# Kernel optimization log

Measured on AMD Instinct MI355X. Metric: run time of the kernel, lower is better.

The kernel has to match this reference:

```python
import jax, jax.numpy as jnp
import numpy as np

B, T, I, H, L, O = 32, 512, 256, 512, 2, 128

def setup_inputs() -> dict:
    key = jax.random.key(0)
    ks = jax.random.split(key, 11)
    s_i = 1.0 / np.sqrt(H)
    inp = {"x": jax.random.normal(ks[0], (B, T, I), jnp.float32)}
    for l in range(L):
        in_dim = I if l == 0 else H
        inp[f"W_ih_{l}"] = jax.random.uniform(ks[1 + 4 * l], (3 * H, in_dim), jnp.float32, -s_i, s_i)
        inp[f"W_hh_{l}"] = jax.random.uniform(ks[2 + 4 * l], (3 * H, H), jnp.float32, -s_i, s_i)
        inp[f"b_ih_{l}"] = jax.random.uniform(ks[3 + 4 * l], (3 * H,), jnp.float32, -s_i, s_i)
        inp[f"b_hh_{l}"] = jax.random.uniform(ks[4 + 4 * l], (3 * H,), jnp.float32, -s_i, s_i)
    inp["fc_W"] = jax.random.uniform(ks[9], (O, H), jnp.float32, -s_i, s_i)
    inp["fc_b"] = jax.random.uniform(ks[10], (O,), jnp.float32, -s_i, s_i)
    return inp

def _gru_layer(x, W_ih, W_hh, b_ih, b_hh):
    # x: [B,T,in] -> precompute input projections once (big batched GEMM)
    xp = jnp.einsum('bti,gi->btg', x, W_ih) + b_ih  # [B,T,3H]
    h0 = jnp.zeros((x.shape[0], W_hh.shape[1]), x.dtype)
    def step(h, xt):  # xt: [B,3H]
        gh = h @ W_hh.T + b_hh  # [B,3H]
        xr, xz, xn = jnp.split(xt, 3, axis=-1)
        hr, hz, hn = jnp.split(gh, 3, axis=-1)
        r = jax.nn.sigmoid(xr + hr)
        z = jax.nn.sigmoid(xz + hz)
        n = jnp.tanh(xn + r * hn)
        h_new = (1.0 - z) * n + z * h
        return h_new, h_new
    hT, ys = jax.lax.scan(step, h0, jnp.swapaxes(xp, 0, 1))  # ys: [T,B,H]
    return jnp.swapaxes(ys, 0, 1), hT

def reference(x, W_ih_0, W_hh_0, b_ih_0, b_hh_0, W_ih_1, W_hh_1, b_ih_1, b_hh_1, fc_W, fc_b):
    layers = [(W_ih_0, W_hh_0, b_ih_0, b_hh_0), (W_ih_1, W_hh_1, b_ih_1, b_hh_1)]
    h = x
    finals = []
    for (Wi, Wh, bi, bh) in layers:
        h, hT = _gru_layer(h, Wi, Wh, bi, bh)
        finals.append(hT)
    hidden = jnp.stack(finals, axis=0)  # [L,B,H]
    out = jnp.einsum('bth,oh->bto', h, fc_W) + fc_b  # [B,T,O]
    return out, hidden
```

## Files before the change

### kernel.cpp

```cpp
#include <hip/hip_runtime.h>
#include <math.h>

#define Bsz 32
#define Tt  512
#define Isz 256
#define Hsz 512
#define G3  1536
#define Osz 128

#define NBLK 256
#define TPB  512
#define G0_L0 1u
#define G0_L1 4096u
#define POLL_GUARD (1 << 22)

typedef float f4  __attribute__((ext_vector_type(4)));
typedef float f32x4 __attribute__((ext_vector_type(4)));
typedef _Float16 half8_t __attribute__((ext_vector_type(8)));
typedef _Float16 half4_t __attribute__((ext_vector_type(4)));
typedef unsigned int u32;
typedef u32 u32x2 __attribute__((ext_vector_type(2)));

__device__ __forceinline__ float sigf(float x) { return 1.0f / (1.0f + expf(-x)); }

__global__ void f32_to_f16(const float* __restrict__ in, _Float16* __restrict__ out, int n4) {
    int i = threadIdx.x + blockIdx.x * blockDim.x;
    int stride = blockDim.x * gridDim.x;
    for (int k = i; k < n4; k += stride) {
        float4 v = reinterpret_cast<const float4*>(in)[k];
        half4_t o;
        o[0] = (_Float16)v.x; o[1] = (_Float16)v.y;
        o[2] = (_Float16)v.z; o[3] = (_Float16)v.w;
        reinterpret_cast<half4_t*>(out)[k] = o;
    }
}

__global__ void init_pbuf(u32x2* pbuf, u32 gen0) {
    int i = threadIdx.x + blockIdx.x * blockDim.x;
    const int n = Bsz * Hsz;
    for (; i < n; i += gridDim.x * blockDim.x) {
        pbuf[i]     = (u32x2){0u, gen0};
        pbuf[n + i] = (u32x2){0u, 0u};
    }
}

__global__ void __launch_bounds__(TPB, 2) gru_rec(
    const float* __restrict__ xp,
    const float* __restrict__ Whh,
    const float* __restrict__ bhh,
    float* __restrict__ hall,
    u32x2* __restrict__ pbuf,
    float* __restrict__ hid_out,
    u32 g0)
{
    const int tid = threadIdx.x;
    const int b   = blockIdx.x & 31;
    const int p   = blockIdx.x >> 5;
    const int jl  = tid >> 3;
    const int kc  = tid & 7;
    const int j   = p * 64 + jl;

    __shared__ float hsh[8 * 68];

    f4 wreg[3][16];
    #pragma unroll
    for (int g = 0; g < 3; ++g) {
        const float* wp = Whh + (size_t)(g * Hsz + j) * Hsz + kc * 64;
        #pragma unroll
        for (int q = 0; q < 16; ++q)
            wreg[g][q] = *reinterpret_cast<const f4*>(wp + q * 4);
    }
    #pragma unroll
    for (int g = 0; g < 3; ++g)
        #pragma unroll
        for (int q = 0; q < 16; ++q)
            asm volatile("" : "+v"(wreg[g][q]));

    const float bh0 = bhh[0 * Hsz + j];
    const float bh1 = bhh[1 * Hsz + j];
    const float bh2 = bhh[2 * Hsz + j];

    for (int t = 0; t < Tt; ++t) {
        const u32 rg = g0 + (u32)t;
        const u32 wg = rg + 1u;
        const u32x2* src = pbuf + (size_t)(t & 1) * (Bsz * Hsz) + b * Hsz;
        u32x2*       dst = pbuf + (size_t)((t + 1) & 1) * (Bsz * Hsz) + b * Hsz;

        float xr = 0.f, xz = 0.f, xn = 0.f;
        if (kc == 0) {
            const float* pp = xp + (size_t)(b * Tt + t) * G3;
            xr = pp[j];
            xz = pp[Hsz + j];
            xn = pp[2 * Hsz + j];
        }

        {
            const u32x2* sp = src + tid;
            int guard = 0;
            for (;;) {
                u32x2 pr;
                asm volatile("global_load_dwordx2 %0, %1, off sc0 sc1\n\t"
                             "s_waitcnt vmcnt(0)"
                             : "=&v"(pr) : "v"(sp) : "memory");
                if (__all(pr[1] == rg) || ++guard > POLL_GUARD) {
                    hsh[(tid >> 6) * 68 + (tid & 63)] = __uint_as_float(pr[0]);
                    break;
                }
                __builtin_amdgcn_s_sleep(1);
            }
        }
        __syncthreads();

        float a0 = 0.f, a1 = 0.f, a2 = 0.f;
        {
            const f4* hp = reinterpret_cast<const f4*>(hsh) + kc * 17;
            #pragma unroll
            for (int q = 0; q < 16; ++q) {
                f4 hv4 = hp[q];
                a0 = fmaf(wreg[0][q][0], hv4[0], a0);
                a0 = fmaf(wreg[0][q][1], hv4[1], a0);
                a0 = fmaf(wreg[0][q][2], hv4[2], a0);
                a0 = fmaf(wreg[0][q][3], hv4[3], a0);
                a1 = fmaf(wreg[1][q][0], hv4[0], a1);
                a1 = fmaf(wreg[1][q][1], hv4[1], a1);
                a1 = fmaf(wreg[1][q][2], hv4[2], a1);
                a1 = fmaf(wreg[1][q][3], hv4[3], a1);
                a2 = fmaf(wreg[2][q][0], hv4[0], a2);
                a2 = fmaf(wreg[2][q][1], hv4[1], a2);
                a2 = fmaf(wreg[2][q][2], hv4[2], a2);
                a2 = fmaf(wreg[2][q][3], hv4[3], a2);
            }
        }

        #pragma unroll
        for (int off = 1; off < 8; off <<= 1) {
            a0 += __shfl_xor(a0, off, 64);
            a1 += __shfl_xor(a1, off, 64);
            a2 += __shfl_xor(a2, off, 64);
        }

        if (kc == 0) {
            float rr = sigf(xr + a0 + bh0);
            float zz = sigf(xz + a1 + bh1);
            float nn = tanhf(xn + rr * (a2 + bh2));
            float ho = hsh[(j >> 6) * 68 + (j & 63)];
            float hv = (1.0f - zz) * nn + zz * ho;
            u32x2 pk = (u32x2){__float_as_uint(hv), wg};
            asm volatile("global_store_dwordx2 %0, %1, off sc0 sc1"
                         :: "v"(dst + j), "v"(pk) : "memory");
            hall[(size_t)(b * Tt + t) * Hsz + j] = hv;
            if (t == Tt - 1) hid_out[b * Hsz + j] = hv;
        }

        __syncthreads();
    }
}

__global__ void __launch_bounds__(256) gemm_nt_mfma(
    const float* __restrict__ A,
    const _Float16* __restrict__ Wh,
    const float* __restrict__ bias,
    float* __restrict__ C,
    int M, int N, int K)
{
    const int tid = threadIdx.x;
    const int l   = tid & 63;
    const int w   = tid >> 6;
    const int wm  = w >> 1, wn = w & 1;
    const int m0  = blockIdx.y * 128 + wm * 64;
    const int n0  = blockIdx.x * 128 + wn * 64;
    const int lr  = l & 15;
    const int lk  = (l >> 4) * 8;

    f32x4 acc[4][4];
    #pragma unroll
    for (int mt = 0; mt < 4; ++mt)
        #pragma unroll
        for (int nt = 0; nt < 4; ++nt)
            acc[mt][nt] = (f32x4){0.f, 0.f, 0.f, 0.f};

    for (int ks = 0; ks < K; ks += 32) {
        half8_t af[4], bf[4];
        #pragma unroll
        for (int mt = 0; mt < 4; ++mt) {
            const float* pa = A + (size_t)(m0 + mt * 16 + lr) * K + ks + lk;
            float4 v0 = *reinterpret_cast<const float4*>(pa);
            float4 v1 = *reinterpret_cast<const float4*>(pa + 4);
            half8_t h;
            h[0] = (_Float16)v0.x; h[1] = (_Float16)v0.y;
            h[2] = (_Float16)v0.z; h[3] = (_Float16)v0.w;
            h[4] = (_Float16)v1.x; h[5] = (_Float16)v1.y;
            h[6] = (_Float16)v1.z; h[7] = (_Float16)v1.w;
            af[mt] = h;
        }
        #pragma unroll
        for (int nt = 0; nt < 4; ++nt)
            bf[nt] = *reinterpret_cast<const half8_t*>(Wh + (size_t)(n0 + nt * 16 + lr) * K + ks + lk);
        #pragma unroll
        for (int mt = 0; mt < 4; ++mt)
            #pragma unroll
            for (int nt = 0; nt < 4; ++nt)
                acc[mt][nt] = __builtin_amdgcn_mfma_f32_16x16x32_f16(af[mt], bf[nt], acc[mt][nt], 0, 0, 0);
    }

    #pragma unroll
    for (int nt = 0; nt < 4; ++nt) {
        const int colg = n0 + nt * 16 + lr;
        const float bb = bias[colg];
        #pragma unroll
        for (int mt = 0; mt < 4; ++mt) {
            #pragma unroll
            for (int r = 0; r < 4; ++r) {
                int rowg = m0 + mt * 16 + (l >> 4) * 4 + r;
                C[(size_t)rowg * N + colg] = acc[mt][nt][r] + bb;
            }
        }
    }
}

#define GM 64
#define GN 64
#define GK 16
__global__ void __launch_bounds__(256) gemm_nt_bias(
    const float* __restrict__ A, const float* __restrict__ W,
    const float* __restrict__ bias, float* __restrict__ C,
    int M, int N, int K)
{
    __shared__ float As[GK][GM];
    __shared__ float Bs[GK][GN];
    const int tid = threadIdx.x;
    const int n0 = blockIdx.x * GN;
    const int m0 = blockIdx.y * GM;
    const int tn = tid & 15;
    const int tm = tid >> 4;
    const int lrow = tid >> 2;
    const int lkq  = tid & 3;

    float acc[4][4];
    #pragma unroll
    for (int i = 0; i < 4; ++i)
        #pragma unroll
        for (int jj = 0; jj < 4; ++jj) acc[i][jj] = 0.0f;

    for (int k0 = 0; k0 < K; k0 += GK) {
        float4 av = *reinterpret_cast<const float4*>(&A[(size_t)(m0 + lrow) * K + k0 + lkq * 4]);
        float4 wv = *reinterpret_cast<const float4*>(&W[(size_t)(n0 + lrow) * K + k0 + lkq * 4]);
        __syncthreads();
        As[lkq * 4 + 0][lrow] = av.x; As[lkq * 4 + 1][lrow] = av.y;
        As[lkq * 4 + 2][lrow] = av.z; As[lkq * 4 + 3][lrow] = av.w;
        Bs[lkq * 4 + 0][lrow] = wv.x; Bs[lkq * 4 + 1][lrow] = wv.y;
        Bs[lkq * 4 + 2][lrow] = wv.z; Bs[lkq * 4 + 3][lrow] = wv.w;
        __syncthreads();
        #pragma unroll
        for (int k = 0; k < GK; ++k) {
            float4 a4 = *reinterpret_cast<const float4*>(&As[k][tm * 4]);
            float4 b4 = *reinterpret_cast<const float4*>(&Bs[k][tn * 4]);
            acc[0][0] = fmaf(a4.x, b4.x, acc[0][0]); acc[0][1] = fmaf(a4.x, b4.y, acc[0][1]);
            acc[0][2] = fmaf(a4.x, b4.z, acc[0][2]); acc[0][3] = fmaf(a4.x, b4.w, acc[0][3]);
            acc[1][0] = fmaf(a4.y, b4.x, acc[1][0]); acc[1][1] = fmaf(a4.y, b4.y, acc[1][1]);
            acc[1][2] = fmaf(a4.y, b4.z, acc[1][2]); acc[1][3] = fmaf(a4.y, b4.w, acc[1][3]);
            acc[2][0] = fmaf(a4.z, b4.x, acc[2][0]); acc[2][1] = fmaf(a4.z, b4.y, acc[2][1]);
            acc[2][2] = fmaf(a4.z, b4.z, acc[2][2]); acc[2][3] = fmaf(a4.z, b4.w, acc[2][3]);
            acc[3][0] = fmaf(a4.w, b4.x, acc[3][0]); acc[3][1] = fmaf(a4.w, b4.y, acc[3][1]);
            acc[3][2] = fmaf(a4.w, b4.z, acc[3][2]); acc[3][3] = fmaf(a4.w, b4.w, acc[3][3]);
        }
    }

    float4 bb = *reinterpret_cast<const float4*>(&bias[n0 + tn * 4]);
    #pragma unroll
    for (int i = 0; i < 4; ++i) {
        int m = m0 + tm * 4 + i;
        float4 o;
        o.x = acc[i][0] + bb.x; o.y = acc[i][1] + bb.y;
        o.z = acc[i][2] + bb.z; o.w = acc[i][3] + bb.w;
        *reinterpret_cast<float4*>(&C[(size_t)m * N + n0 + tn * 4]) = o;
    }
}

extern "C" void kernel_launch(void* const* d_in, const int* in_sizes, int n_in,
                              void* d_out, int out_size, void* d_ws, size_t ws_size,
                              hipStream_t stream) {
    (void)in_sizes; (void)n_in; (void)out_size; (void)ws_size;
    const float* x    = (const float*)d_in[0];
    const float* Wih0 = (const float*)d_in[1];
    const float* Whh0 = (const float*)d_in[2];
    const float* bih0 = (const float*)d_in[3];
    const float* bhh0 = (const float*)d_in[4];
    const float* Wih1 = (const float*)d_in[5];
    const float* Whh1 = (const float*)d_in[6];
    const float* bih1 = (const float*)d_in[7];
    const float* bhh1 = (const float*)d_in[8];
    const float* fcW  = (const float*)d_in[9];
    const float* fcb  = (const float*)d_in[10];

    float* out = (float*)d_out;
    float* hid = out + (size_t)Bsz * Tt * Osz;

    char* ws = (char*)d_ws;
    const size_t xp_off   = 0;
    const size_t hall_off = xp_off + (size_t)Bsz * Tt * G3 * 4;
    const size_t pbuf_off = hall_off + (size_t)Bsz * Tt * Hsz * 4;
    const size_t w0h_off  = pbuf_off + (size_t)2 * Bsz * Hsz * 8;
    const size_t w1h_off  = w0h_off + (size_t)G3 * Isz * 2;
    float*     xp    = (float*)(ws + xp_off);
    float*     hall  = (float*)(ws + hall_off);
    u32x2*     pbuf  = (u32x2*)(ws + pbuf_off);
    _Float16*  W0h   = (_Float16*)(ws + w0h_off);
    _Float16*  W1h   = (_Float16*)(ws + w1h_off);

    hipLaunchKernelGGL(f32_to_f16, dim3(128), dim3(256), 0, stream, Wih0, W0h, G3 * Isz / 4);
    hipLaunchKernelGGL(f32_to_f16, dim3(256), dim3(256), 0, stream, Wih1, W1h, G3 * Hsz / 4);

    hipLaunchKernelGGL(gemm_nt_mfma, dim3(G3 / 128, (Bsz * Tt) / 128), dim3(256), 0, stream,
                       x, W0h, bih0, xp, Bsz * Tt, G3, Isz);

    hipLaunchKernelGGL(init_pbuf, dim3(64), dim3(256), 0, stream, pbuf, G0_L0);
    hipLaunchKernelGGL(gru_rec, dim3(NBLK), dim3(TPB), 0, stream,
                       xp, Whh0, bhh0, hall, pbuf, hid, G0_L0);

    hipLaunchKernelGGL(gemm_nt_mfma, dim3(G3 / 128, (Bsz * Tt) / 128), dim3(256), 0, stream,
                       hall, W1h, bih1, xp, Bsz * Tt, G3, Hsz);

    hipLaunchKernelGGL(init_pbuf, dim3(64), dim3(256), 0, stream, pbuf, G0_L1);
    hipLaunchKernelGGL(gru_rec, dim3(NBLK), dim3(TPB), 0, stream,
                       xp, Whh1, bhh1, hall, pbuf, hid + Bsz * Hsz, G0_L1);

    hipLaunchKernelGGL(gemm_nt_bias, dim3(Osz / GN, (Bsz * Tt) / GM), dim3(256), 0, stream,
                       hall, fcW, fcb, out, Bsz * Tt, Osz, Hsz);
}
```

Baseline: 1.978 ms.

## Process two batch rows per block with half the hidden slice

```diff
diff --git a/kernel.cpp b/kernel.cpp
--- a/kernel.cpp
+++ b/kernel.cpp
@@ -13,6 +13,7 @@
 #define G0_L0 1u
 #define G0_L1 4096u
 #define POLL_GUARD (1 << 22)
+#define CH 36
 
 typedef float f4  __attribute__((ext_vector_type(4)));
 typedef float f32x4 __attribute__((ext_vector_type(4)));
@@ -53,57 +54,66 @@
     float* __restrict__ hid_out,
     u32 g0)
 {
-    const int tid = threadIdx.x;
-    const int b   = blockIdx.x & 31;
-    const int p   = blockIdx.x >> 5;
-    const int jl  = tid >> 3;
-    const int kc  = tid & 7;
-    const int j   = p * 64 + jl;
-
-    __shared__ float hsh[8 * 68];
-
-    f4 wreg[3][16];
+    const int tid  = threadIdx.x;
+    const int pr   = blockIdx.x & 15;
+    const int p    = blockIdx.x >> 4;
+    const int b1   = pr * 2;
+    const int b2   = b1 + 1;
+    const int jl   = tid >> 4;
+    const int kc   = tid & 15;
+    const int j    = p * 32 + jl;
+    const int BH   = Bsz * Hsz;
+
+    __shared__ float hA[16 * CH];
+    __shared__ float hB[16 * CH];
+
+    f4 wreg[3][8];
     #pragma unroll
     for (int g = 0; g < 3; ++g) {
-        const float* wp = Whh + (size_t)(g * Hsz + j) * Hsz + kc * 64;
-        #pragma unroll
-        for (int q = 0; q < 16; ++q)
+        const float* wp = Whh + (size_t)(g * Hsz + j) * Hsz + kc * 32;
+        #pragma unroll
+        for (int q = 0; q < 8; ++q)
             wreg[g][q] = *reinterpret_cast<const f4*>(wp + q * 4);
     }
     #pragma unroll
     for (int g = 0; g < 3; ++g)
         #pragma unroll
-        for (int q = 0; q < 16; ++q)
+        for (int q = 0; q < 8; ++q)
             asm volatile("" : "+v"(wreg[g][q]));
 
     const float bh0 = bhh[0 * Hsz + j];
     const float bh1 = bhh[1 * Hsz + j];
     const float bh2 = bhh[2 * Hsz + j];
 
+    const int li = (tid >> 5) * CH + (tid & 31);
+    const int lo = (j >> 5) * CH + (j & 31);
+
     for (int t = 0; t < Tt; ++t) {
         const u32 rg = g0 + (u32)t;
         const u32 wg = rg + 1u;
-        const u32x2* src = pbuf + (size_t)(t & 1) * (Bsz * Hsz) + b * Hsz;
-        u32x2*       dst = pbuf + (size_t)((t + 1) & 1) * (Bsz * Hsz) + b * Hsz;
-
-        float xr = 0.f, xz = 0.f, xn = 0.f;
+        const u32x2* srcA = pbuf + (size_t)(t & 1) * BH + b1 * Hsz;
+        u32x2*       dstA = pbuf + (size_t)((t + 1) & 1) * BH + b1 * Hsz;
+        const u32x2* srcB = pbuf + (size_t)(t & 1) * BH + b2 * Hsz;
+        u32x2*       dstB = pbuf + (size_t)((t + 1) & 1) * BH + b2 * Hsz;
+
+        float xrA = 0.f, xzA = 0.f, xnA = 0.f, xrB = 0.f, xzB = 0.f, xnB = 0.f;
         if (kc == 0) {
-            const float* pp = xp + (size_t)(b * Tt + t) * G3;
-            xr = pp[j];
-            xz = pp[Hsz + j];
-            xn = pp[2 * Hsz + j];
+            const float* pA = xp + (size_t)(b1 * Tt + t) * G3;
+            const float* pB = xp + (size_t)(b2 * Tt + t) * G3;
+            xrA = pA[j]; xzA = pA[Hsz + j]; xnA = pA[2 * Hsz + j];
+            xrB = pB[j]; xzB = pB[Hsz + j]; xnB = pB[2 * Hsz + j];
         }
 
         {
-            const u32x2* sp = src + tid;
+            const u32x2* sp = srcA + tid;
             int guard = 0;
             for (;;) {
-                u32x2 pr;
+                u32x2 prv;
                 asm volatile("global_load_dwordx2 %0, %1, off sc0 sc1\n\t"
                              "s_waitcnt vmcnt(0)"
-                             : "=&v"(pr) : "v"(sp) : "memory");
-                if (__all(pr[1] == rg) || ++guard > POLL_GUARD) {
-                    hsh[(tid >> 6) * 68 + (tid & 63)] = __uint_as_float(pr[0]);
+                             : "=&v"(prv) : "v"(sp) : "memory");
+                if (__all(prv[1] == rg) || ++guard > POLL_GUARD) {
+                    hA[li] = __uint_as_float(prv[0]);
                     break;
                 }
                 __builtin_amdgcn_s_sleep(1);
@@ -111,11 +121,11 @@
         }
         __syncthreads();
 
-        float a0 = 0.f, a1 = 0.f, a2 = 0.f;
         {
-            const f4* hp = reinterpret_cast<const f4*>(hsh) + kc * 17;
-            #pragma unroll
-            for (int q = 0; q < 16; ++q) {
+            float a0 = 0.f, a1 = 0.f, a2 = 0.f;
+            const f4* hp = reinterpret_cast<const f4*>(hA + kc * CH);
+            #pragma unroll
+            for (int q = 0; q < 8; ++q) {
                 f4 hv4 = hp[q];
                 a0 = fmaf(wreg[0][q][0], hv4[0], a0);
                 a0 = fmaf(wreg[0][q][1], hv4[1], a0);
@@ -130,29 +140,81 @@
                 a2 = fmaf(wreg[2][q][2], hv4[2], a2);
                 a2 = fmaf(wreg[2][q][3], hv4[3], a2);
             }
-        }
-
-        #pragma unroll
-        for (int off = 1; off < 8; off <<= 1) {
-            a0 += __shfl_xor(a0, off, 64);
-            a1 += __shfl_xor(a1, off, 64);
-            a2 += __shfl_xor(a2, off, 64);
-        }
-
-        if (kc == 0) {
-            float rr = sigf(xr + a0 + bh0);
-            float zz = sigf(xz + a1 + bh1);
-            float nn = tanhf(xn + rr * (a2 + bh2));
-            float ho = hsh[(j >> 6) * 68 + (j & 63)];
-            float hv = (1.0f - zz) * nn + zz * ho;
-            u32x2 pk = (u32x2){__float_as_uint(hv), wg};
-            asm volatile("global_store_dwordx2 %0, %1, off sc0 sc1"
-                         :: "v"(dst + j), "v"(pk) : "memory");
-            hall[(size_t)(b * Tt + t) * Hsz + j] = hv;
-            if (t == Tt - 1) hid_out[b * Hsz + j] = hv;
-        }
-
+            #pragma unroll
+            for (int off = 1; off < 16; off <<= 1) {
+                a0 += __shfl_xor(a0, off, 64);
+                a1 += __shfl_xor(a1, off, 64);
+                a2 += __shfl_xor(a2, off, 64);
+            }
+            if (kc == 0) {
+                float rr = sigf(xrA + a0 + bh0);
+                float zz = sigf(xzA + a1 + bh1);
+                float nn = tanhf(xnA + rr * (a2 + bh2));
+                float ho = hA[lo];
+                float hv = (1.0f - zz) * nn + zz * ho;
+                u32x2 pk = (u32x2){__float_as_uint(hv), wg};
+                asm volatile("global_store_dwordx2 %0, %1, off sc0 sc1"
+                             :: "v"(dstA + j), "v"(pk) : "memory");
+                hall[(size_t)(b1 * Tt + t) * Hsz + j] = hv;
+                if (t == Tt - 1) hid_out[b1 * Hsz + j] = hv;
+            }
+        }
+
+        {
+            const u32x2* sp = srcB + tid;
+            int guard = 0;
+            for (;;) {
+                u32x2 prv;
+                asm volatile("global_load_dwordx2 %0, %1, off sc0 sc1\n\t"
+                             "s_waitcnt vmcnt(0)"
+                             : "=&v"(prv) : "v"(sp) : "memory");
+                if (__all(prv[1] == rg) || ++guard > POLL_GUARD) {
+                    hB[li] = __uint_as_float(prv[0]);
+                    break;
+                }
+                __builtin_amdgcn_s_sleep(1);
+            }
+        }
         __syncthreads();
+
+        {
+            float a0 = 0.f, a1 = 0.f, a2 = 0.f;
+            const f4* hp = reinterpret_cast<const f4*>(hB + kc * CH);
+            #pragma unroll
+            for (int q = 0; q < 8; ++q) {
+                f4 hv4 = hp[q];
+                a0 = fmaf(wreg[0][q][0], hv4[0], a0);
+                a0 = fmaf(wreg[0][q][1], hv4[1], a0);
+                a0 = fmaf(wreg[0][q][2], hv4[2], a0);
+                a0 = fmaf(wreg[0][q][3], hv4[3], a0);
+                a1 = fmaf(wreg[1][q][0], hv4[0], a1);
+                a1 = fmaf(wreg[1][q][1], hv4[1], a1);
+                a1 = fmaf(wreg[1][q][2], hv4[2], a1);
+                a1 = fmaf(wreg[1][q][3], hv4[3], a1);
+                a2 = fmaf(wreg[2][q][0], hv4[0], a2);
+                a2 = fmaf(wreg[2][q][1], hv4[1], a2);
+                a2 = fmaf(wreg[2][q][2], hv4[2], a2);
+                a2 = fmaf(wreg[2][q][3], hv4[3], a2);
+            }
+            #pragma unroll
+            for (int off = 1; off < 16; off <<= 1) {
+                a0 += __shfl_xor(a0, off, 64);
+                a1 += __shfl_xor(a1, off, 64);
+                a2 += __shfl_xor(a2, off, 64);
+            }
+            if (kc == 0) {
+                float rr = sigf(xrB + a0 + bh0);
+                float zz = sigf(xzB + a1 + bh1);
+                float nn = tanhf(xnB + rr * (a2 + bh2));
+                float ho = hB[lo];
+                float hv = (1.0f - zz) * nn + zz * ho;
+                u32x2 pk = (u32x2){__float_as_uint(hv), wg};
+                asm volatile("global_store_dwordx2 %0, %1, off sc0 sc1"
+                             :: "v"(dstB + j), "v"(pk) : "memory");
+                hall[(size_t)(b2 * Tt + t) * Hsz + j] = hv;
+                if (t == Tt - 1) hid_out[b2 * Hsz + j] = hv;
+            }
+        }
     }
 }
 
```

Measured after the change: 3.033 ms. 53.4% more time.

## Fuse both GRU layers into one wavefront-pipelined persistent kernel

Applied to the files above, without the earlier changes.

```diff
diff --git a/kernel.cpp b/kernel.cpp
--- a/kernel.cpp
+++ b/kernel.cpp
@@ -8,18 +8,19 @@
 #define G3  1536
 #define Osz 128
 
-#define NBLK 256
 #define TPB  512
-#define G0_L0 1u
-#define G0_L1 4096u
+#define NFUSED 192
 #define POLL_GUARD (1 << 22)
-
-typedef float f4  __attribute__((ext_vector_type(4)));
+#define BH  (Bsz * Hsz)
+#define XQP (Bsz * G3)
+
+typedef float f4 __attribute__((ext_vector_type(4)));
 typedef float f32x4 __attribute__((ext_vector_type(4)));
 typedef _Float16 half8_t __attribute__((ext_vector_type(8)));
 typedef _Float16 half4_t __attribute__((ext_vector_type(4)));
 typedef unsigned int u32;
 typedef u32 u32x2 __attribute__((ext_vector_type(2)));
+typedef u32 u32x4 __attribute__((ext_vector_type(4)));
 
 __device__ __forceinline__ float sigf(float x) { return 1.0f / (1.0f + expf(-x)); }
 
@@ -35,132 +36,397 @@
     }
 }
 
-__global__ void init_pbuf(u32x2* pbuf, u32 gen0) {
+__global__ void init_bufs(u32x2* pbuf0, u32x2* pbuf1, u32x2* xqbuf,
+                          int* prog0, int* prog1) {
     int i = threadIdx.x + blockIdx.x * blockDim.x;
-    const int n = Bsz * Hsz;
-    for (; i < n; i += gridDim.x * blockDim.x) {
-        pbuf[i]     = (u32x2){0u, gen0};
-        pbuf[n + i] = (u32x2){0u, 0u};
+    int stride = blockDim.x * gridDim.x;
+    for (int k = i; k < 8 * BH; k += stride)
+        pbuf0[k] = (k < BH) ? (u32x2){0u, 1u} : (u32x2){0u, 0u};
+    for (int k = i; k < 2 * BH; k += stride)
+        pbuf1[k] = (k < BH) ? (u32x2){0u, 1u} : (u32x2){0u, 0u};
+    for (int k = i; k < 8 * XQP; k += stride)
+        xqbuf[k] = (u32x2){0u, 0u};
+    for (int k = i; k < 1024; k += stride) { prog0[k] = 0; prog1[k] = 0; }
+}
+
+__global__ void __launch_bounds__(TPB, 1) gru_fused(
+    const float* __restrict__ xp,
+    const float* __restrict__ Whh0, const float* __restrict__ bhh0,
+    const float* __restrict__ Wih1, const float* __restrict__ bih1,
+    const float* __restrict__ Whh1, const float* __restrict__ bhh1,
+    float* __restrict__ hall,
+    u32x2* __restrict__ pbuf0,
+    u32x2* __restrict__ pbuf1,
+    u32x2* __restrict__ xqbuf,
+    int* __restrict__ prog0,
+    int* __restrict__ prog1,
+    float* __restrict__ hid)
+{
+    const int tid  = threadIdx.x;
+    const int rid  = blockIdx.x;
+    const int role = rid >> 6;
+    const int loc  = rid & 63;
+    const int bg   = loc >> 3;
+    const int p    = loc & 7;
+    const int jl   = tid >> 3;
+    const int kc   = tid & 7;
+    const int j    = p * 64 + jl;
+    const int li   = (tid >> 6) * 68 + (tid & 63);
+    const int lo   = (j >> 6) * 68 + (j & 63);
+
+    __shared__ float hs[4 * 544];
+
+    if (role == 0) {
+        f4 w[3][16];
+        #pragma unroll
+        for (int g = 0; g < 3; ++g) {
+            const float* wp = Whh0 + (size_t)(g * Hsz + j) * Hsz + kc * 64;
+            #pragma unroll
+            for (int q = 0; q < 16; ++q) w[g][q] = *reinterpret_cast<const f4*>(wp + q * 4);
+        }
+        #pragma unroll
+        for (int g = 0; g < 3; ++g)
+            #pragma unroll
+            for (int q = 0; q < 16; ++q) asm volatile("" : "+v"(w[g][q]));
+        const float b0 = bhh0[j], b1 = bhh0[Hsz + j], b2 = bhh0[2 * Hsz + j];
+        int bpk = 0;
+
+        for (int t = 0; t < Tt; ++t) {
+            const u32 rg = (u32)(t + 1), wgen = rg + 1u;
+            const u32x2* src = pbuf0 + (size_t)(t & 7) * BH + bg * 4 * Hsz;
+            u32x2*       dst = pbuf0 + (size_t)((t + 1) & 7) * BH + bg * 4 * Hsz;
+
+            float xr[4], xz[4], xn[4];
+            if (kc == 0) {
+                #pragma unroll
+                for (int bi = 0; bi < 4; ++bi) {
+                    const float* pp = xp + (size_t)((bg * 4 + bi) * Tt + t) * G3;
+                    xr[bi] = pp[j]; xz[bi] = pp[Hsz + j]; xn[bi] = pp[2 * Hsz + j];
+                }
+            }
+
+            {
+                const u32x2* a0 = src + 0 * Hsz + tid;
+                const u32x2* a1 = src + 1 * Hsz + tid;
+                const u32x2* a2 = src + 2 * Hsz + tid;
+                const u32x2* a3 = src + 3 * Hsz + tid;
+                u32x2 r0, r1, r2, r3;
+                int guard = 0;
+                for (;;) {
+                    asm volatile(
+                        "global_load_dwordx2 %0, %4, off sc0 sc1\n\t"
+                        "global_load_dwordx2 %1, %5, off sc0 sc1\n\t"
+                        "global_load_dwordx2 %2, %6, off sc0 sc1\n\t"
+                        "global_load_dwordx2 %3, %7, off sc0 sc1\n\t"
+                        "s_waitcnt vmcnt(0)"
+                        : "=&v"(r0), "=&v"(r1), "=&v"(r2), "=&v"(r3)
+                        : "v"(a0), "v"(a1), "v"(a2), "v"(a3) : "memory");
+                    bool ok = (r0[1] == rg) && (r1[1] == rg) && (r2[1] == rg) && (r3[1] == rg);
+                    if (__all(ok) || ++guard > POLL_GUARD) break;
+                    __builtin_amdgcn_s_sleep(1);
+                }
+                hs[0 * 544 + li] = __uint_as_float(r0[0]);
+                hs[1 * 544 + li] = __uint_as_float(r1[0]);
+                hs[2 * 544 + li] = __uint_as_float(r2[0]);
+                hs[3 * 544 + li] = __uint_as_float(r3[0]);
+            }
+            __syncthreads();
+
+            {
+                const int thr = t - 7;
+                if (tid < 64 && thr > bpk) {
+                    const int* pp = prog0 + ((bg << 3) + (tid & 7)) * 16;
+                    int guard = 0;
+                    for (;;) {
+                        int v;
+                        asm volatile("global_load_dword %0, %1, off sc0 sc1\n\t"
+                                     "s_waitcnt vmcnt(0)" : "=&v"(v) : "v"(pp) : "memory");
+                        int mv = (tid < 8) ? v : 0x7fffffff;
+                        #pragma unroll
+                        for (int off = 1; off < 8; off <<= 1) {
+                            int o = __shfl_xor(mv, off, 64);
+                            mv = (o < mv) ? o : mv;
+                        }
+                        mv = __shfl(mv, 0, 64);
+                        if (mv >= thr || ++guard > POLL_GUARD) { bpk = mv; break; }
+                        __builtin_amdgcn_s_sleep(2);
+                    }
+                }
+            }
+            __syncthreads();
+
+            #pragma unroll
+            for (int bi = 0; bi < 4; ++bi) {
+                float a0 = 0.f, a1 = 0.f, a2 = 0.f;
+                const f4* hp = reinterpret_cast<const f4*>(hs + bi * 544) + kc * 17;
+                #pragma unroll
+                for (int q = 0; q < 16; ++q) {
+                    f4 hv4 = hp[q];
+                    a0 = fmaf(w[0][q][0], hv4[0], a0); a0 = fmaf(w[0][q][1], hv4[1], a0);
+                    a0 = fmaf(w[0][q][2], hv4[2], a0); a0 = fmaf(w[0][q][3], hv4[3], a0);
+                    a1 = fmaf(w[1][q][0], hv4[0], a1); a1 = fmaf(w[1][q][1], hv4[1], a1);
+                    a1 = fmaf(w[1][q][2], hv4[2], a1); a1 = fmaf(w[1][q][3], hv4[3], a1);
+                    a2 = fmaf(w[2][q][0], hv4[0], a2); a2 = fmaf(w[2][q][1], hv4[1], a2);
+                    a2 = fmaf(w[2][q][2], hv4[2], a2); a2 = fmaf(w[2][q][3], hv4[3], a2);
+                }
+                #pragma unroll
+                for (int off = 1; off < 8; off <<= 1) {
+                    a0 += __shfl_xor(a0, off, 64);
+                    a1 += __shfl_xor(a1, off, 64);
+                    a2 += __shfl_xor(a2, off, 64);
+                }
+                if (kc == 0) {
+                    float rr = sigf(xr[bi] + a0 + b0);
+                    float zz = sigf(xz[bi] + a1 + b1);
+                    float nn = tanhf(xn[bi] + rr * (a2 + b2));
+                    float ho = hs[bi * 544 + lo];
+                    float hv = (1.0f - zz) * nn + zz * ho;
+                    u32x2 pk = (u32x2){__float_as_uint(hv), wgen};
+                    asm volatile("global_store_dwordx2 %0, %1, off sc0 sc1"
+                                 :: "v"(dst + bi * Hsz + j), "v"(pk) : "memory");
+                    if (t == Tt - 1) hid[(bg * 4 + bi) * Hsz + j] = hv;
+                }
+            }
+            __syncthreads();
+        }
+    } else if (role == 1) {
+        f4 w[3][16];
+        #pragma unroll
+        for (int g = 0; g < 3; ++g) {
+            const float* wp = Wih1 + (size_t)(g * Hsz + j) * Hsz + kc * 64;
+            #pragma unroll
+            for (int q = 0; q < 16; ++q) w[g][q] = *reinterpret_cast<const f4*>(wp + q * 4);
+        }
+        #pragma unroll
+        for (int g = 0; g < 3; ++g)
+            #pragma unroll
+            for (int q = 0; q < 16; ++q) asm volatile("" : "+v"(w[g][q]));
+        const float b0 = bih1[j], b1 = bih1[Hsz + j], b2 = bih1[2 * Hsz + j];
+        int bpk = 0;
+
+        for (int t = 0; t < Tt; ++t) {
+            const u32 rgp = (u32)(t + 2);
+            const u32x2* src = pbuf0 + (size_t)((t + 1) & 7) * BH + bg * 4 * Hsz;
+            u32x2* xdst = xqbuf + (size_t)((t + 1) & 7) * XQP;
+
+            {
+                const u32x2* a0 = src + 0 * Hsz + tid;
+                const u32x2* a1 = src + 1 * Hsz + tid;
+                const u32x2* a2 = src + 2 * Hsz + tid;
+                const u32x2* a3 = src + 3 * Hsz + tid;
+                u32x2 r0, r1, r2, r3;
+                int guard = 0;
+                for (;;) {
+                    asm volatile(
+                        "global_load_dwordx2 %0, %4, off sc0 sc1\n\t"
+                        "global_load_dwordx2 %1, %5, off sc0 sc1\n\t"
+                        "global_load_dwordx2 %2, %6, off sc0 sc1\n\t"
+                        "global_load_dwordx2 %3, %7, off sc0 sc1\n\t"
+                        "s_waitcnt vmcnt(0)"
+                        : "=&v"(r0), "=&v"(r1), "=&v"(r2), "=&v"(r3)
+                        : "v"(a0), "v"(a1), "v"(a2), "v"(a3) : "memory");
+                    bool ok = (r0[1] == rgp) && (r1[1] == rgp) && (r2[1] == rgp) && (r3[1] == rgp);
+                    if (__all(ok) || ++guard > POLL_GUARD) break;
+                    __builtin_amdgcn_s_sleep(1);
+                }
+                hs[0 * 544 + li] = __uint_as_float(r0[0]);
+                hs[1 * 544 + li] = __uint_as_float(r1[0]);
+                hs[2 * 544 + li] = __uint_as_float(r2[0]);
+                hs[3 * 544 + li] = __uint_as_float(r3[0]);
+            }
+            __syncthreads();
+
+            if (tid == 0) {
+                int pv = t + 1;
+                asm volatile("global_store_dword %0, %1, off sc0 sc1"
+                             :: "v"(prog0 + ((bg << 3) + p) * 16), "v"(pv) : "memory");
+                const int thr = t - 7;
+                if (thr > bpk) {
+                    const int* pp = prog1 + ((bg << 3) + p) * 16;
+                    int guard = 0;
+                    for (;;) {
+                        int v;
+                        asm volatile("global_load_dword %0, %1, off sc0 sc1\n\t"
+                                     "s_waitcnt vmcnt(0)" : "=&v"(v) : "v"(pp) : "memory");
+                        if (v >= thr || ++guard > POLL_GUARD) { bpk = v; break; }
+                        __builtin_amdgcn_s_sleep(2);
+                    }
+                }
+            }
+            __syncthreads();
+
+            #pragma unroll
+            for (int bi = 0; bi < 4; ++bi) {
+                float a0 = 0.f, a1 = 0.f, a2 = 0.f;
+                const f4* hp = reinterpret_cast<const f4*>(hs + bi * 544) + kc * 17;
+                #pragma unroll
+                for (int q = 0; q < 16; ++q) {
+                    f4 hv4 = hp[q];
+                    a0 = fmaf(w[0][q][0], hv4[0], a0); a0 = fmaf(w[0][q][1], hv4[1], a0);
+                    a0 = fmaf(w[0][q][2], hv4[2], a0); a0 = fmaf(w[0][q][3], hv4[3], a0);
+                    a1 = fmaf(w[1][q][0], hv4[0], a1); a1 = fmaf(w[1][q][1], hv4[1], a1);
+                    a1 = fmaf(w[1][q][2], hv4[2], a1); a1 = fmaf(w[1][q][3], hv4[3], a1);
+                    a2 = fmaf(w[2][q][0], hv4[0], a2); a2 = fmaf(w[2][q][1], hv4[1], a2);
+                    a2 = fmaf(w[2][q][2], hv4[2], a2); a2 = fmaf(w[2][q][3], hv4[3], a2);
+                }
+                #pragma unroll
+                for (int off = 1; off < 8; off <<= 1) {
+                    a0 += __shfl_xor(a0, off, 64);
+                    a1 += __shfl_xor(a1, off, 64);
+                    a2 += __shfl_xor(a2, off, 64);
+                }
+                if (kc == 0) {
+                    float v0 = a0 + b0, v1 = a1 + b1, v2 = a2 + b2;
+                    u32x4 pk0 = (u32x4){__float_as_uint(v0), rgp, __float_as_uint(v1), rgp};
+                    u32x2 pk1 = (u32x2){__float_as_uint(v2), rgp};
+                    u32x2* xa = xdst + (size_t)((bg * 4 + bi) * Hsz + j) * 3;
+                    asm volatile(
+                        "global_store_dwordx4 %0, %1, off sc0 sc1\n\t"
+                        "global_store_dwordx2 %0, %2, off offset:16 sc0 sc1"
+                        :: "v"(xa), "v"(pk0), "v"(pk1) : "memory");
+                }
+            }
+            __syncthreads();
+        }
+    } else {
+        f4 w[3][16];
+        #pragma unroll
+        for (int g = 0; g < 3; ++g) {
+            const float* wp = Whh1 + (size_t)(g * Hsz + j) * Hsz + kc * 64;
+            #pragma unroll
+            for (int q = 0; q < 16; ++q) w[g][q] = *reinterpret_cast<const f4*>(wp + q * 4);
+        }
+        #pragma unroll
+        for (int g = 0; g < 3; ++g)
+            #pragma unroll
+            for (int q = 0; q < 16; ++q) asm volatile("" : "+v"(w[g][q]));
+        const float b0 = bhh1[j], b1 = bhh1[Hsz + j], b2 = bhh1[2 * Hsz + j];
+
+        for (int t = 0; t < Tt; ++t) {
+            const u32 rg = (u32)(t + 1), wgen = rg + 1u, rgx = rg + 1u;
+            const u32x2* src = pbuf1 + (size_t)(t & 1) * BH + bg * 4 * Hsz;
+            u32x2*       dst = pbuf1 + (size_t)((t + 1) & 1) * BH + bg * 4 * Hsz;
+            const u32x2* xsrc = xqbuf + (size_t)((t + 1) & 7) * XQP;
+
+            u32x4 xa_[4]; u32x2 xb_[4];
+            const u32x2* xaddr[4];
+            #pragma unroll
+            for (int bi = 0; bi < 4; ++bi)
+                xaddr[bi] = xsrc + (size_t)((bg * 4 + bi) * Hsz + j) * 3;
+            if (kc == 0) {
+                #pragma unroll
+                for (int bi = 0; bi < 4; ++bi)
+                    asm volatile(
+                        "global_load_dwordx4 %0, %2, off sc0 sc1\n\t"
+                        "global_load_dwordx2 %1, %2, off offset:16 sc0 sc1"
+                        : "=&v"(xa_[bi]), "=&v"(xb_[bi]) : "v"(xaddr[bi]) : "memory");
+            }
+
+            {
+                const u32x2* a0 = src + 0 * Hsz + tid;
+                const u32x2* a1 = src + 1 * Hsz + tid;
+                const u32x2* a2 = src + 2 * Hsz + tid;
+                const u32x2* a3 = src + 3 * Hsz + tid;
+                u32x2 r0, r1, r2, r3;
+                int guard = 0;
+                for (;;) {
+                    asm volatile(
+                        "global_load_dwordx2 %0, %4, off sc0 sc1\n\t"
+                        "global_load_dwordx2 %1, %5, off sc0 sc1\n\t"
+                        "global_load_dwordx2 %2, %6, off sc0 sc1\n\t"
+                        "global_load_dwordx2 %3, %7, off sc0 sc1\n\t"
+                        "s_waitcnt vmcnt(0)"
+                        : "=&v"(r0), "=&v"(r1), "=&v"(r2), "=&v"(r3)
+                        : "v"(a0), "v"(a1), "v"(a2), "v"(a3) : "memory");
+                    bool ok = (r0[1] == rg) && (r1[1] == rg) && (r2[1] == rg) && (r3[1] == rg);
+                    if (__all(ok) || ++guard > POLL_GUARD) break;
+                    __builtin_amdgcn_s_sleep(1);
+                }
+                hs[0 * 544 + li] = __uint_as_float(r0[0]);
+                hs[1 * 544 + li] = __uint_as_float(r1[0]);
+                hs[2 * 544 + li] = __uint_as_float(r2[0]);
+                hs[3 * 544 + li] = __uint_as_float(r3[0]);
+            }
+
+            {
+                int guard = 0;
+                for (;;) {
+                    asm volatile("s_waitcnt vmcnt(0)"
+                                 : "+v"(xa_[0]), "+v"(xb_[0]), "+v"(xa_[1]), "+v"(xb_[1]),
+                                   "+v"(xa_[2]), "+v"(xb_[2]), "+v"(xa_[3]), "+v"(xb_[3])
+                                 :: "memory");
+                    bool okx = true;
+                    if (kc == 0) {
+                        #pragma unroll
+                        for (int bi = 0; bi < 4; ++bi)
+                            okx = okx && (xa_[bi][1] == rgx) && (xa_[bi][3] == rgx)
+                                      && (xb_[bi][1] == rgx);
+                    }
+                    bool c = (kc != 0) || okx;
+                    if (__all(c) || ++guard > POLL_GUARD) break;
+                    if (kc == 0) {
+                        #pragma unroll
+                        for (int bi = 0; bi < 4; ++bi)
+                            asm volatile(
+                                "global_load_dwordx4 %0, %2, off sc0 sc1\n\t"
+                                "global_load_dwordx2 %1, %2, off offset:16 sc0 sc1"
+                                : "=&v"(xa_[bi]), "=&v"(xb_[bi]) : "v"(xaddr[bi]) : "memory");
+                    }
+                    __builtin_amdgcn_s_sleep(1);
+                }
+            }
+            __syncthreads();
+
+            if (tid == 0) {
+                int pv = t + 1;
+                asm volatile("global_store_dword %0, %1, off sc0 sc1"
+                             :: "v"(prog1 + ((bg << 3) + p) * 16), "v"(pv) : "memory");
+            }
+
+            #pragma unroll
+            for (int bi = 0; bi < 4; ++bi) {
+                float g0 = 0.f, g1 = 0.f, g2 = 0.f;
+                const f4* hp = reinterpret_cast<const f4*>(hs + bi * 544) + kc * 17;
+                #pragma unroll
+                for (int q = 0; q < 16; ++q) {
+                    f4 hv4 = hp[q];
+                    g0 = fmaf(w[0][q][0], hv4[0], g0); g0 = fmaf(w[0][q][1], hv4[1], g0);
+                    g0 = fmaf(w[0][q][2], hv4[2], g0); g0 = fmaf(w[0][q][3], hv4[3], g0);
+                    g1 = fmaf(w[1][q][0], hv4[0], g1); g1 = fmaf(w[1][q][1], hv4[1], g1);
+                    g1 = fmaf(w[1][q][2], hv4[2], g1); g1 = fmaf(w[1][q][3], hv4[3], g1);
+                    g2 = fmaf(w[2][q][0], hv4[0], g2); g2 = fmaf(w[2][q][1], hv4[1], g2);
+                    g2 = fmaf(w[2][q][2], hv4[2], g2); g2 = fmaf(w[2][q][3], hv4[3], g2);
+                }
+                #pragma unroll
+                for (int off = 1; off < 8; off <<= 1) {
+                    g0 += __shfl_xor(g0, off, 64);
+                    g1 += __shfl_xor(g1, off, 64);
+                    g2 += __shfl_xor(g2, off, 64);
+                }
+                if (kc == 0) {
+                    float xr = __uint_as_float(xa_[bi][0]);
+                    float xz = __uint_as_float(xa_[bi][2]);
+                    float xn = __uint_as_float(xb_[bi][0]);
+                    float rr = sigf(xr + g0 + b0);
+                    float zz = sigf(xz + g1 + b1);
+                    float nn = tanhf(xn + rr * (g2 + b2));
+                    float ho = hs[bi * 544 + lo];
+                    float hv = (1.0f - zz) * nn + zz * ho;
+                    u32x2 pk = (u32x2){__float_as_uint(hv), wgen};
+                    asm volatile("global_store_dwordx2 %0, %1, off sc0 sc1"
+                                 :: "v"(dst + bi * Hsz + j), "v"(pk) : "memory");
+                    hall[(size_t)((bg * 4 + bi) * Tt + t) * Hsz + j] = hv;
+                    if (t == Tt - 1) hid[BH + (bg * 4 + bi) * Hsz + j] = hv;
+                }
+            }
+            __syncthreads();
+        }
     }
 }
 
-__global__ void __launch_bounds__(TPB, 2) gru_rec(
-    const float* __restrict__ xp,
-    const float* __restrict__ Whh,
-    const float* __restrict__ bhh,
-    float* __restrict__ hall,
-    u32x2* __restrict__ pbuf,
-    float* __restrict__ hid_out,
-    u32 g0)
-{
-    const int tid = threadIdx.x;
-    const int b   = blockIdx.x & 31;
-    const int p   = blockIdx.x >> 5;
-    const int jl  = tid >> 3;
-    const int kc  = tid & 7;
-    const int j   = p * 64 + jl;
-
-    __shared__ float hsh[8 * 68];
-
-    f4 wreg[3][16];
-    #pragma unroll
-    for (int g = 0; g < 3; ++g) {
-        const float* wp = Whh + (size_t)(g * Hsz + j) * Hsz + kc * 64;
-        #pragma unroll
-        for (int q = 0; q < 16; ++q)
-            wreg[g][q] = *reinterpret_cast<const f4*>(wp + q * 4);
-    }
-    #pragma unroll
-    for (int g = 0; g < 3; ++g)
-        #pragma unroll
-        for (int q = 0; q < 16; ++q)
-            asm volatile("" : "+v"(wreg[g][q]));
-
-    const float bh0 = bhh[0 * Hsz + j];
-    const float bh1 = bhh[1 * Hsz + j];
-    const float bh2 = bhh[2 * Hsz + j];
-
-    for (int t = 0; t < Tt; ++t) {
-        const u32 rg = g0 + (u32)t;
-        const u32 wg = rg + 1u;
-        const u32x2* src = pbuf + (size_t)(t & 1) * (Bsz * Hsz) + b * Hsz;
-        u32x2*       dst = pbuf + (size_t)((t + 1) & 1) * (Bsz * Hsz) + b * Hsz;
-
-        float xr = 0.f, xz = 0.f, xn = 0.f;
-        if (kc == 0) {
-            const float* pp = xp + (size_t)(b * Tt + t) * G3;
-            xr = pp[j];
-            xz = pp[Hsz + j];
-            xn = pp[2 * Hsz + j];
-        }
-
-        {
-            const u32x2* sp = src + tid;
-            int guard = 0;
-            for (;;) {
-                u32x2 pr;
-                asm volatile("global_load_dwordx2 %0, %1, off sc0 sc1\n\t"
-                             "s_waitcnt vmcnt(0)"
-                             : "=&v"(pr) : "v"(sp) : "memory");
-                if (__all(pr[1] == rg) || ++guard > POLL_GUARD) {
-                    hsh[(tid >> 6) * 68 + (tid & 63)] = __uint_as_float(pr[0]);
-                    break;
-                }
-                __builtin_amdgcn_s_sleep(1);
-            }
-        }
-        __syncthreads();
-
-        float a0 = 0.f, a1 = 0.f, a2 = 0.f;
-        {
-            const f4* hp = reinterpret_cast<const f4*>(hsh) + kc * 17;
-            #pragma unroll
-            for (int q = 0; q < 16; ++q) {
-                f4 hv4 = hp[q];
-                a0 = fmaf(wreg[0][q][0], hv4[0], a0);
-                a0 = fmaf(wreg[0][q][1], hv4[1], a0);
-                a0 = fmaf(wreg[0][q][2], hv4[2], a0);
-                a0 = fmaf(wreg[0][q][3], hv4[3], a0);
-                a1 = fmaf(wreg[1][q][0], hv4[0], a1);
-                a1 = fmaf(wreg[1][q][1], hv4[1], a1);
-                a1 = fmaf(wreg[1][q][2], hv4[2], a1);
-                a1 = fmaf(wreg[1][q][3], hv4[3], a1);
-                a2 = fmaf(wreg[2][q][0], hv4[0], a2);
-                a2 = fmaf(wreg[2][q][1], hv4[1], a2);
-                a2 = fmaf(wreg[2][q][2], hv4[2], a2);
-                a2 = fmaf(wreg[2][q][3], hv4[3], a2);
-            }
-        }
-
-        #pragma unroll
-        for (int off = 1; off < 8; off <<= 1) {
-            a0 += __shfl_xor(a0, off, 64);
-            a1 += __shfl_xor(a1, off, 64);
-            a2 += __shfl_xor(a2, off, 64);
-        }
-
-        if (kc == 0) {
-            float rr = sigf(xr + a0 + bh0);
-            float zz = sigf(xz + a1 + bh1);
-            float nn = tanhf(xn + rr * (a2 + bh2));
-            float ho = hsh[(j >> 6) * 68 + (j & 63)];
-            float hv = (1.0f - zz) * nn + zz * ho;
-            u32x2 pk = (u32x2){__float_as_uint(hv), wg};
-            asm volatile("global_store_dwordx2 %0, %1, off sc0 sc1"
-                         :: "v"(dst + j), "v"(pk) : "memory");
-            hall[(size_t)(b * Tt + t) * Hsz + j] = hv;
-            if (t == Tt - 1) hid_out[b * Hsz + j] = hv;
-        }
-
-        __syncthreads();
-    }
-}
-
 __global__ void __launch_bounds__(256) gemm_nt_mfma(
-    const float* __restrict__ A,
-    const _Float16* __restrict__ Wh,
-    const float* __restrict__ bias,
-    float* __restrict__ C,
+    const float* __restrict__ A, const _Float16* __restrict__ Wh,
+    const float* __restrict__ bias, float* __restrict__ C,
     int M, int N, int K)
 {
     const int tid = threadIdx.x;
@@ -297,33 +563,32 @@
     float* hid = out + (size_t)Bsz * Tt * Osz;
 
     char* ws = (char*)d_ws;
-    const size_t xp_off   = 0;
-    const size_t hall_off = xp_off + (size_t)Bsz * Tt * G3 * 4;
-    const size_t pbuf_off = hall_off + (size_t)Bsz * Tt * Hsz * 4;
-    const size_t w0h_off  = pbuf_off + (size_t)2 * Bsz * Hsz * 8;
-    const size_t w1h_off  = w0h_off + (size_t)G3 * Isz * 2;
+    const size_t xp_off    = 0;
+    const size_t hall_off  = xp_off + (size_t)Bsz * Tt * G3 * 4;
+    const size_t pbuf0_off = hall_off + (size_t)Bsz * Tt * Hsz * 4;
+    const size_t pbuf1_off = pbuf0_off + (size_t)8 * BH * 8;
+    const size_t xq_off    = pbuf1_off + (size_t)2 * BH * 8;
+    const size_t w0h_off   = xq_off + (size_t)8 * XQP * 8;
+    const size_t prog0_off = w0h_off + (size_t)G3 * Isz * 2;
+    const size_t prog1_off = prog0_off + 4096;
     float*     xp    = (float*)(ws + xp_off);
     float*     hall  = (float*)(ws + hall_off);
-    u32x2*     pbuf  = (u32x2*)(ws + pbuf_off);
+    u32x2*     pbuf0 = (u32x2*)(ws + pbuf0_off);
+    u32x2*     pbuf1 = (u32x2*)(ws + pbuf1_off);
+    u32x2*     xqbuf = (u32x2*)(ws + xq_off);
     _Float16*  W0h   = (_Float16*)(ws + w0h_off);
-    _Float16*  W1h   = (_Float16*)(ws + w1h_off);
+    int*       prog0 = (int*)(ws + prog0_off);
+    int*       prog1 = (int*)(ws + prog1_off);
 
     hipLaunchKernelGGL(f32_to_f16, dim3(128), dim3(256), 0, stream, Wih0, W0h, G3 * Isz / 4);
-    hipLaunchKernelGGL(f32_to_f16, dim3(256), dim3(256), 0, stream, Wih1, W1h, G3 * Hsz / 4);
-
     hipLaunchKernelGGL(gemm_nt_mfma, dim3(G3 / 128, (Bsz * Tt) / 128), dim3(256), 0, stream,
                        x, W0h, bih0, xp, Bsz * Tt, G3, Isz);
 
-    hipLaunchKernelGGL(init_pbuf, dim3(64), dim3(256), 0, stream, pbuf, G0_L0);
-    hipLaunchKernelGGL(gru_rec, dim3(NBLK), dim3(TPB), 0, stream,
-                       xp, Whh0, bhh0, hall, pbuf, hid, G0_L0);
-
-    hipLaunchKernelGGL(gemm_nt_mfma, dim3(G3 / 128, (Bsz * Tt) / 128), dim3(256), 0, stream,
-                       hall, W1h, bih1, xp, Bsz * Tt, G3, Hsz);
-
-    hipLaunchKernelGGL(init_pbuf, dim3(64), dim3(256), 0, stream, pbuf, G0_L1);
-    hipLaunchKernelGGL(gru_rec, dim3(NBLK), dim3(TPB), 0, stream,
-                       xp, Whh1, bhh1, hall, pbuf, hid + Bsz * Hsz, G0_L1);
+    hipLaunchKernelGGL(init_bufs, dim3(128), dim3(256), 0, stream,
+                       pbuf0, pbuf1, xqbuf, prog0, prog1);
+    hipLaunchKernelGGL(gru_fused, dim3(NFUSED), dim3(TPB), 0, stream,
+                       xp, Whh0, bhh0, Wih1, bih1, Whh1, bhh1,
+                       hall, pbuf0, pbuf1, xqbuf, prog0, prog1, hid);
 
     hipLaunchKernelGGL(gemm_nt_bias, dim3(Osz / GN, (Bsz * Tt) / GM), dim3(256), 0, stream,
                        hall, fcW, fcb, out, Bsz * Tt, Osz, Hsz);
```

Result: slower. 3.162 ms (+59.9%).
